# Kernel tuning notes

Hardware: AMD Instinct MI355X
Metric: run time of the kernel (lower is better)

## Reference

```python
import jax, jax.numpy as jnp
import numpy as np

INPUT_SIZE = 84 * 84 * 4  # 28224
FEATURE_SIZE = 1500
BATCH = 256

def setup_inputs() -> dict:
    key = jax.random.key(0)
    k_x, k_we, k_wd = jax.random.split(key, 3)
    scale_e = 1.0 / np.sqrt(INPUT_SIZE)
    scale_d = 1.0 / np.sqrt(FEATURE_SIZE)
    return {
        "x": jax.random.normal(k_x, (BATCH, INPUT_SIZE), dtype=jnp.float32),
        "W_enc": jax.random.normal(k_we, (FEATURE_SIZE, INPUT_SIZE), dtype=jnp.float32) * scale_e,
        "b_enc": jnp.zeros((FEATURE_SIZE,), dtype=jnp.float32),
        "W_dec": jax.random.normal(k_wd, (INPUT_SIZE, FEATURE_SIZE), dtype=jnp.float32) * scale_d,
        "b_dec": jnp.zeros((INPUT_SIZE,), dtype=jnp.float32),
    }

def reference(x, W_enc, b_enc, W_dec, b_dec):
    # Encoder: y_enc = sigmoid(x @ W_enc^T + b_enc), shape [B, F]
    y_enc = jax.nn.sigmoid(jnp.einsum('bi,fi->bf', x, W_enc) + b_enc)
    # Contractive (Jacobian Frobenius norm) term, closed form:
    # d y_enc[b,i] / d x[b,:] = y*(1-y) * W_enc[i,:]
    # jac_reg = sum_{b,i} (y*(1-y))^2 * ||W_enc[i,:]||^2
    s2 = jnp.square(y_enc * (1.0 - y_enc))          # [B, F]
    row_norm2 = jnp.sum(jnp.square(W_enc), axis=1)  # [F]
    jac_reg = jnp.sum(s2 * row_norm2)               # scalar
    # Decoder
    y_out = jax.nn.sigmoid(jnp.einsum('bf,if->bi', y_enc, W_dec) + b_dec)
    return y_out, jac_reg
```

## Files before the change

### kernel.cpp

```cpp
#include <hip/hip_runtime.h>
#include <hip/hip_bf16.h>


#define BATCH 256
#define IN    28224
#define FEAT  1500
#define FPAD  1536
#define KPAD  1504
#define ENC_S 21

typedef __attribute__((ext_vector_type(8))) short short8;
typedef __attribute__((ext_vector_type(4))) float f32x4;

__device__ __forceinline__ unsigned pack2(float lo, float hi) {
    unsigned a = __float_as_uint(lo) + 0x8000u;
    unsigned b = __float_as_uint(hi) + 0x8000u;
    return __builtin_amdgcn_perm(b, a, 0x07060302);
}
__device__ __forceinline__ unsigned short f2bf(float f) {
    unsigned u = __float_as_uint(f);
    return (unsigned short)((u + 0x7FFFu + ((u >> 16) & 1u)) >> 16);
}

__device__ __forceinline__ void async16(const unsigned short* g, unsigned short* l) {
    __builtin_amdgcn_global_load_lds(
        (const __attribute__((address_space(1))) unsigned int*)g,
        (__attribute__((address_space(3))) unsigned int*)l,
        16, 0, 0);
}


__global__ __launch_bounds__(256) void cvt_x(const float* __restrict__ x,
                                             unsigned short* __restrict__ xbf) {
    int idx = blockIdx.x * 256 + threadIdx.x;
    float4 v = ((const float4*)x)[idx];
    ((uint2*)xbf)[idx] = make_uint2(pack2(v.x, v.y), pack2(v.z, v.w));
}


__global__ __launch_bounds__(256) void enc_fused(const unsigned short* __restrict__ xbf,
                                                 const float* __restrict__ We,
                                                 float* __restrict__ part,
                                                 float* __restrict__ rn2) {
    __shared__ unsigned short As[256 * 32];
    __shared__ unsigned short Bs[64 * 32];

    const int n0 = blockIdx.x * 64;
    const int kb = blockIdx.y * 1344;
    const int t    = threadIdx.x;
    const int lane = t & 63;
    const int w    = t >> 6;
    const int l15  = lane & 15;
    const int quad = lane >> 4;

    const unsigned short* ga = xbf + (long)(w * 64 + (lane >> 2)) * IN + kb + (lane & 3) * 8;
    unsigned short* la = As + (w * 64) * 32;

    const int br = t >> 2;
    const int bf_ = n0 + br;
    const bool bvalid = bf_ < FEAT;
    const float* bsrc = We + (long)(bvalid ? bf_ : FEAT - 1) * IN + kb + (t & 3) * 8;
    unsigned short* bdst = Bs + br * 32 + (t & 3) * 8;

    float rsq = 0.f;
    f32x4 acc[4][4];
#pragma unroll
    for (int mt = 0; mt < 4; ++mt)
#pragma unroll
        for (int nt = 0; nt < 4; ++nt) { f32x4 z = {0.f,0.f,0.f,0.f}; acc[mt][nt] = z; }

    float4 v0 = *(const float4*)(bsrc);
    float4 v1 = *(const float4*)(bsrc + 4);

    for (int k = 0; k < 1344; k += 32) {
        __syncthreads();
        async16(ga + k,            la);
        async16(ga + 16 * IN + k,  la + 16 * 32);
        async16(ga + 32 * IN + k,  la + 32 * 32);
        async16(ga + 48 * IN + k,  la + 48 * 32);
        uint2 p0 = make_uint2(pack2(v0.x, v0.y), pack2(v0.z, v0.w));
        uint2 p1 = make_uint2(pack2(v1.x, v1.y), pack2(v1.z, v1.w));
        if (!bvalid) { p0 = make_uint2(0u, 0u); p1 = make_uint2(0u, 0u); }
        *(uint2*)bdst       = p0;
        *(uint2*)(bdst + 4) = p1;
        rsq += v0.x*v0.x + v0.y*v0.y + v0.z*v0.z + v0.w*v0.w
             + v1.x*v1.x + v1.y*v1.y + v1.z*v1.z + v1.w*v1.w;
        const int kn = k + 32;
        if (kn < 1344) {
            v0 = *(const float4*)(bsrc + kn);
            v1 = *(const float4*)(bsrc + kn + 4);
        }
        __syncthreads();

        short8 a[4], b[4];
#pragma unroll
        for (int mt = 0; mt < 4; ++mt)
            a[mt] = *(const short8*)(As + (w * 64 + mt * 16 + l15) * 32 + quad * 8);
#pragma unroll
        for (int nt = 0; nt < 4; ++nt)
            b[nt] = *(const short8*)(Bs + (nt * 16 + l15) * 32 + quad * 8);
#pragma unroll
        for (int mt = 0; mt < 4; ++mt)
#pragma unroll
            for (int nt = 0; nt < 4; ++nt)
                acc[mt][nt] = __builtin_amdgcn_mfma_f32_16x16x32_bf16(a[mt], b[nt], acc[mt][nt], 0, 0, 0);
    }

    float* ps = part + (long)blockIdx.y * (BATCH * FPAD);
#pragma unroll
    for (int nt = 0; nt < 4; ++nt) {
        const int col = n0 + nt * 16 + l15;
#pragma unroll
        for (int mt = 0; mt < 4; ++mt) {
            const int row = w * 64 + mt * 16 + quad * 4;
#pragma unroll
            for (int r = 0; r < 4; ++r)
                ps[(long)(row + r) * FPAD + col] = acc[mt][nt][r];
        }
    }

    rsq += __shfl_xor(rsq, 1);
    rsq += __shfl_xor(rsq, 2);
    if ((lane & 3) == 0 && bvalid) atomicAdd(&rn2[bf_], rsq);
}

__global__ __launch_bounds__(256) void act_jac_f(const float* __restrict__ part,
                                                 const float* __restrict__ be,
                                                 const float* __restrict__ rn2,
                                                 unsigned short* __restrict__ yenc,
                                                 float* __restrict__ jac) {
    const int b = blockIdx.y;
    const int f = blockIdx.x * 256 + threadIdx.x;
    float local = 0.0f;
    unsigned short h = 0;
    if (f < FEAT) {
        float p = be[f];
#pragma unroll 3
        for (int s = 0; s < ENC_S; ++s)
            p += part[(long)(s * BATCH + b) * FPAD + f];
        float y = 1.0f / (1.0f + __expf(-p));
        h = f2bf(y);
        float sg = y * (1.0f - y);
        local = sg * sg * rn2[f];
    }
    if (f < KPAD) yenc[b * KPAD + f] = h;

    float v = local;
#pragma unroll
    for (int off = 32; off > 0; off >>= 1) v += __shfl_down(v, off);
    __shared__ float red[4];
    if ((threadIdx.x & 63) == 0) red[threadIdx.x >> 6] = v;
    __syncthreads();
    if (threadIdx.x == 0) atomicAdd(jac, red[0] + red[1] + red[2] + red[3]);
}

__global__ __launch_bounds__(256) void dec_fused(const unsigned short* __restrict__ yenc,
                                                 const float* __restrict__ Wd,
                                                 const float* __restrict__ bd,
                                                 float* __restrict__ out) {
    __shared__ unsigned short As[256 * 32];
    __shared__ unsigned short Bs[64 * 32];

    const int n0 = blockIdx.x * 64;
    const int t    = threadIdx.x;
    const int lane = t & 63;
    const int w    = t >> 6;
    const int l15  = lane & 15;
    const int quad = lane >> 4;

    const unsigned short* ga = yenc + (long)(w * 64 + (lane >> 2)) * KPAD + (lane & 3) * 8;
    unsigned short* la = As + (w * 64) * 32;

    const int br = t >> 2;
    const int bn = n0 + br;
    const float* bsrc = Wd + (long)bn * FEAT + (t & 3) * 8;
    unsigned short* bdst = Bs + br * 32 + (t & 3) * 8;

    f32x4 acc[4][4];
#pragma unroll
    for (int mt = 0; mt < 4; ++mt)
#pragma unroll
        for (int nt = 0; nt < 4; ++nt) { f32x4 z = {0.f,0.f,0.f,0.f}; acc[mt][nt] = z; }

    float4 v0 = *(const float4*)(bsrc);
    float4 v1 = *(const float4*)(bsrc + 4);

    for (int k = 0; k < KPAD; k += 32) {
        __syncthreads();
        async16(ga + k,              la);
        async16(ga + 16 * KPAD + k,  la + 16 * 32);
        async16(ga + 32 * KPAD + k,  la + 32 * 32);
        async16(ga + 48 * KPAD + k,  la + 48 * 32);
        *(uint2*)bdst       = make_uint2(pack2(v0.x, v0.y), pack2(v0.z, v0.w));
        *(uint2*)(bdst + 4) = make_uint2(pack2(v1.x, v1.y), pack2(v1.z, v1.w));
        const int kn = k + 32;
        if (kn < KPAD) {
            v0 = *(const float4*)(bsrc + kn);
            const int cc = kn + (t & 3) * 8 + 4;
            if (cc + 3 < FEAT) v1 = *(const float4*)(bsrc + kn + 4);
            else               v1 = make_float4(0.f, 0.f, 0.f, 0.f);
        }
        __syncthreads();

        short8 a[4], b[4];
#pragma unroll
        for (int mt = 0; mt < 4; ++mt)
            a[mt] = *(const short8*)(As + (w * 64 + mt * 16 + l15) * 32 + quad * 8);
#pragma unroll
        for (int nt = 0; nt < 4; ++nt)
            b[nt] = *(const short8*)(Bs + (nt * 16 + l15) * 32 + quad * 8);
#pragma unroll
        for (int mt = 0; mt < 4; ++mt)
#pragma unroll
            for (int nt = 0; nt < 4; ++nt)
                acc[mt][nt] = __builtin_amdgcn_mfma_f32_16x16x32_bf16(a[mt], b[nt], acc[mt][nt], 0, 0, 0);
    }

#pragma unroll
    for (int nt = 0; nt < 4; ++nt) {
        const int col = n0 + nt * 16 + l15;
        const float bias = bd[col];
#pragma unroll
        for (int mt = 0; mt < 4; ++mt) {
            const int row = w * 64 + mt * 16 + quad * 4;
#pragma unroll
            for (int r = 0; r < 4; ++r) {
                float v = acc[mt][nt][r] + bias;
                out[(long)(row + r) * IN + col] = 1.0f / (1.0f + __expf(-v));
            }
        }
    }
}

#define LDA 40

__global__ __launch_bounds__(256) void enc_gemm(const unsigned short* __restrict__ xbf,
                                                const float* __restrict__ We,
                                                float* __restrict__ preact,
                                                float* __restrict__ rn2) {
    __shared__ unsigned short As[256 * LDA];
    __shared__ unsigned short Bs[64 * LDA];
    const int n0 = blockIdx.x * 64;
    const int kb = blockIdx.y * 672;
    const int t = threadIdx.x, lane = t & 63, w = t >> 6, l15 = lane & 15, quad = lane >> 4;
    const unsigned short* asrc = xbf + (long)(t >> 2) * IN + (t & 3) * 8 + kb;
    unsigned short* adst = As + (t >> 2) * LDA + (t & 3) * 8;
    const int brow = t >> 3, bc4 = t & 7;
    const int f0 = n0 + brow, f1 = f0 + 32;
    const float* bsrc0 = We + (long)(f0 < FEAT ? f0 : FEAT - 1) * IN + bc4 * 4 + kb;
    const float* bsrc1 = We + (long)(f1 < FEAT ? f1 : FEAT - 1) * IN + bc4 * 4 + kb;
    unsigned short* bdst0 = Bs + brow * LDA + bc4 * 4;
    unsigned short* bdst1 = bdst0 + 32 * LDA;
    float rsq0 = 0.f, rsq1 = 0.f;
    f32x4 acc[4][4];
#pragma unroll
    for (int mt = 0; mt < 4; ++mt)
#pragma unroll
        for (int nt = 0; nt < 4; ++nt) { f32x4 z = {0.f,0.f,0.f,0.f}; acc[mt][nt] = z; }
    for (int k = 0; k < 672; k += 32) {
        short8 av[4];
#pragma unroll
        for (int j = 0; j < 4; ++j) av[j] = *(const short8*)(asrc + (long)64 * j * IN + k);
        const float4 bv0 = *(const float4*)(bsrc0 + k);
        const float4 bv1 = *(const float4*)(bsrc1 + k);
        __syncthreads();
#pragma unroll
        for (int j = 0; j < 4; ++j) *(short8*)(adst + 64 * j * LDA) = av[j];
        *(uint2*)bdst0 = make_uint2(pack2(bv0.x, bv0.y), pack2(bv0.z, bv0.w));
        *(uint2*)bdst1 = make_uint2(pack2(bv1.x, bv1.y), pack2(bv1.z, bv1.w));
        rsq0 += bv0.x*bv0.x + bv0.y*bv0.y + bv0.z*bv0.z + bv0.w*bv0.w;
        rsq1 += bv1.x*bv1.x + bv1.y*bv1.y + bv1.z*bv1.z + bv1.w*bv1.w;
        __syncthreads();
        short8 a[4], b[4];
#pragma unroll
        for (int mt = 0; mt < 4; ++mt) a[mt] = *(const short8*)(As + (w * 64 + mt * 16 + l15) * LDA + quad * 8);
#pragma unroll
        for (int nt = 0; nt < 4; ++nt) b[nt] = *(const short8*)(Bs + (nt * 16 + l15) * LDA + quad * 8);
#pragma unroll
        for (int mt = 0; mt < 4; ++mt)
#pragma unroll
            for (int nt = 0; nt < 4; ++nt)
                acc[mt][nt] = __builtin_amdgcn_mfma_f32_16x16x32_bf16(a[mt], b[nt], acc[mt][nt], 0, 0, 0);
    }
#pragma unroll
    for (int nt = 0; nt < 4; ++nt) {
        const int col = n0 + nt * 16 + l15;
        if (col < FEAT) {
#pragma unroll
            for (int mt = 0; mt < 4; ++mt) {
                float* p = preact + (long)(w * 64 + mt * 16 + quad * 4) * FEAT + col;
#pragma unroll
                for (int r = 0; r < 4; ++r) atomicAdd(p + (long)r * FEAT, acc[mt][nt][r]);
            }
        }
    }
    {
        float v0 = rsq0, v1 = rsq1;
#pragma unroll
        for (int off = 1; off < 8; off <<= 1) { v0 += __shfl_xor(v0, off); v1 += __shfl_xor(v1, off); }
        if ((lane & 7) == 0) {
            if (f0 < FEAT) atomicAdd(&rn2[f0], v0);
            if (f1 < FEAT) atomicAdd(&rn2[f1], v1);
        }
    }
}

__global__ __launch_bounds__(256) void act_jac(const float* __restrict__ preact,
                                               const float* __restrict__ be,
                                               const float* __restrict__ rn2,
                                               unsigned short* __restrict__ yenc,
                                               float* __restrict__ jac) {
    const int b = blockIdx.y;
    const int f = blockIdx.x * 256 + threadIdx.x;
    float local = 0.0f;
    unsigned short h = 0;
    if (f < FEAT) {
        float p = preact[b * FEAT + f] + be[f];
        float y = 1.0f / (1.0f + __expf(-p));
        h = f2bf(y);
        float s = y * (1.0f - y);
        local = s * s * rn2[f];
    }
    yenc[b * FPAD + f] = h;
    float v = local;
#pragma unroll
    for (int off = 32; off > 0; off >>= 1) v += __shfl_down(v, off);
    __shared__ float red[4];
    if ((threadIdx.x & 63) == 0) red[threadIdx.x >> 6] = v;
    __syncthreads();
    if (threadIdx.x == 0) atomicAdd(jac, red[0] + red[1] + red[2] + red[3]);
}

__global__ __launch_bounds__(256) void dec_gemm(const unsigned short* __restrict__ yenc,
                                                const float* __restrict__ Wd,
                                                const float* __restrict__ bd,
                                                float* __restrict__ out) {
    __shared__ unsigned short As[128 * LDA];
    __shared__ unsigned short Bs[64 * LDA];
    const int m0 = (blockIdx.x & 1) * 128;
    const int n0 = (blockIdx.x >> 1) * 64;
    const int t = threadIdx.x, lane = t & 63, w = t >> 6, l15 = lane & 15, quad = lane >> 4;
    const int mrow = (w >> 1) * 64, ncol = (w & 1) * 32;
    const unsigned short* asrc = yenc + (long)(m0 + (t >> 2)) * FPAD + (t & 3) * 8;
    unsigned short* adst = As + (t >> 2) * LDA + (t & 3) * 8;
    const float* bsrc = Wd + (long)(n0 + (t >> 3)) * FEAT + (t & 7) * 4;
    unsigned short* bdst = Bs + (t >> 3) * LDA + (t & 7) * 4;
    f32x4 acc[4][2];
#pragma unroll
    for (int mt = 0; mt < 4; ++mt)
#pragma unroll
        for (int nt = 0; nt < 2; ++nt) { f32x4 z = {0.f,0.f,0.f,0.f}; acc[mt][nt] = z; }
    for (int k = 0; k < 1504; k += 32) {
        short8 av[2];
#pragma unroll
        for (int j = 0; j < 2; ++j) av[j] = *(const short8*)(asrc + (long)64 * j * FPAD + k);
        float4 bv0, bv1;
        if (k < 1472) {
            bv0 = *(const float4*)(bsrc + k);
            bv1 = *(const float4*)(bsrc + (long)32 * FEAT + k);
        } else {
            if ((t & 7) == 7) { bv0 = make_float4(0,0,0,0); bv1 = bv0; }
            else {
                bv0 = *(const float4*)(bsrc + k);
                bv1 = *(const float4*)(bsrc + (long)32 * FEAT + k);
            }
        }
        __syncthreads();
#pragma unroll
        for (int j = 0; j < 2; ++j) *(short8*)(adst + 64 * j * LDA) = av[j];
        *(uint2*)bdst = make_uint2(pack2(bv0.x, bv0.y), pack2(bv0.z, bv0.w));
        *(uint2*)(bdst + 32 * LDA) = make_uint2(pack2(bv1.x, bv1.y), pack2(bv1.z, bv1.w));
        __syncthreads();
        short8 a[4], b[2];
#pragma unroll
        for (int mt = 0; mt < 4; ++mt) a[mt] = *(const short8*)(As + (mrow + mt * 16 + l15) * LDA + quad * 8);
#pragma unroll
        for (int nt = 0; nt < 2; ++nt) b[nt] = *(const short8*)(Bs + (ncol + nt * 16 + l15) * LDA + quad * 8);
#pragma unroll
        for (int mt = 0; mt < 4; ++mt)
#pragma unroll
            for (int nt = 0; nt < 2; ++nt)
                acc[mt][nt] = __builtin_amdgcn_mfma_f32_16x16x32_bf16(a[mt], b[nt], acc[mt][nt], 0, 0, 0);
    }
#pragma unroll
    for (int nt = 0; nt < 2; ++nt) {
        const int col = n0 + ncol + nt * 16 + l15;
        const float bias = bd[col];
#pragma unroll
        for (int mt = 0; mt < 4; ++mt) {
            const int row = m0 + mrow + mt * 16 + quad * 4;
#pragma unroll
            for (int r = 0; r < 4; ++r) {
                float v = acc[mt][nt][r] + bias;
                out[(long)(row + r) * IN + col] = 1.0f / (1.0f + __expf(-v));
            }
        }
    }
}

extern "C" void kernel_launch(void* const* d_in, const int* in_sizes, int n_in,
                              void* d_out, int out_size, void* d_ws, size_t ws_size,
                              hipStream_t stream) {
    const float* x  = (const float*)d_in[0];
    const float* We = (const float*)d_in[1];
    const float* be = (const float*)d_in[2];
    const float* Wd = (const float*)d_in[3];
    const float* bd = (const float*)d_in[4];
    float* out = (float*)d_out;
    char* ws = (char*)d_ws;

    if (ws_size >= 48257024ull) {
        unsigned short* xbf  = (unsigned short*)ws;
        unsigned short* yenc = (unsigned short*)(ws + 14450688);
        float* part          = (float*)(ws + 15220736);
        float* rn2           = (float*)(ws + 48250880);

        hipMemsetAsync(rn2, 0, 6144, stream);
        hipMemsetAsync(out + 7225344, 0, 4, stream);

        cvt_x<<<7056, 256, 0, stream>>>(x, xbf);
        enc_fused<<<dim3(24, ENC_S), 256, 0, stream>>>(xbf, We, part, rn2);
        act_jac_f<<<dim3(6, 256), 256, 0, stream>>>(part, be, rn2, yenc, out + 7225344);
        dec_fused<<<441, 256, 0, stream>>>(yenc, Wd, bd, out);
    } else {
        float* preact        = (float*)ws;
        float* rn2           = (float*)(ws + 1536000);
        unsigned short* yenc = (unsigned short*)(ws + 1542144);
        unsigned short* xbf  = (unsigned short*)(ws + 2328576);

        hipMemsetAsync(ws, 0, 1542144, stream);
        hipMemsetAsync(out + 7225344, 0, 4, stream);

        cvt_x<<<7056, 256, 0, stream>>>(x, xbf);
        enc_gemm<<<dim3(24, 42), 256, 0, stream>>>(xbf, We, preact, rn2);
        act_jac<<<dim3(6, 256), 256, 0, stream>>>(preact, be, rn2, yenc, out + 7225344);
        dec_gemm<<<882, 256, 0, stream>>>(yenc, Wd, bd, out);
    }
}
```

Before: 462.8 us.

## Double-buffer encoder/decoder GEMM tiles, double split-K, halve decoder M tile

Both fused GEMM kernels move to double-buffered LDS with a k-major layout, so the next tile's loads run alongside the current MFMA work and each iteration needs one barrier instead of two. The encoder split-K factor goes from 21 to 42, giving more blocks for occupancy at the cost of a larger partial-sum buffer and more reduction work in act_jac_f. The decoder splits M into two 128-row halves, which doubles its grid to 882 blocks with smaller per-wave tiles. The fused path now needs a larger workspace, and the old path is used as a fallback when the workspace is too small.

Result: slower. 558.8 us (+20.7%).

```diff
diff --git a/kernel.cpp b/kernel.cpp
--- a/kernel.cpp
+++ b/kernel.cpp
@@ -7,7 +7,7 @@
 #define FEAT  1500
 #define FPAD  1536
 #define KPAD  1504
-#define ENC_S 21
+#define ENC_S 42
 
 typedef __attribute__((ext_vector_type(8))) short short8;
 typedef __attribute__((ext_vector_type(4))) float f32x4;
@@ -38,29 +38,32 @@
 }
 
 
-__global__ __launch_bounds__(256) void enc_fused(const unsigned short* __restrict__ xbf,
-                                                 const float* __restrict__ We,
-                                                 float* __restrict__ part,
-                                                 float* __restrict__ rn2) {
-    __shared__ unsigned short As[256 * 32];
-    __shared__ unsigned short Bs[64 * 32];
+__global__ __launch_bounds__(256, 4) void enc_fused(const unsigned short* __restrict__ xbf,
+                                                    const float* __restrict__ We,
+                                                    float* __restrict__ part,
+                                                    float* __restrict__ rn2) {
+    __shared__ unsigned short As[2 * 4 * 256 * 8];
+    __shared__ unsigned short Bs[2 * 4 * 64 * 8];
 
     const int n0 = blockIdx.x * 64;
-    const int kb = blockIdx.y * 1344;
+    const int kb = blockIdx.y * 672;
     const int t    = threadIdx.x;
     const int lane = t & 63;
     const int w    = t >> 6;
     const int l15  = lane & 15;
     const int quad = lane >> 4;
 
-    const unsigned short* ga = xbf + (long)(w * 64 + (lane >> 2)) * IN + kb + (lane & 3) * 8;
-    unsigned short* la = As + (w * 64) * 32;
-
-    const int br = t >> 2;
+    const unsigned short* gaA = xbf + (long)lane * IN + kb + w * 8;
+    unsigned short* laA = As + w * 2048;
+
+    const int br = t >> 2, sb = t & 3;
     const int bf_ = n0 + br;
     const bool bvalid = bf_ < FEAT;
-    const float* bsrc = We + (long)(bvalid ? bf_ : FEAT - 1) * IN + kb + (t & 3) * 8;
-    unsigned short* bdst = Bs + br * 32 + (t & 3) * 8;
+    const float* bsrc = We + (long)(bvalid ? bf_ : FEAT - 1) * IN + kb + sb * 8;
+    unsigned short* lbB = Bs + sb * 512 + br * 8;
+
+    const unsigned short* rdA = As + quad * 2048 + (w * 64 + l15) * 8;
+    const unsigned short* rdB = Bs + quad * 512 + l15 * 8;
 
     float rsq = 0.f;
     f32x4 acc[4][4];
@@ -71,39 +74,54 @@
 
     float4 v0 = *(const float4*)(bsrc);
     float4 v1 = *(const float4*)(bsrc + 4);
-
-    for (int k = 0; k < 1344; k += 32) {
-        __syncthreads();
-        async16(ga + k,            la);
-        async16(ga + 16 * IN + k,  la + 16 * 32);
-        async16(ga + 32 * IN + k,  la + 32 * 32);
-        async16(ga + 48 * IN + k,  la + 48 * 32);
-        uint2 p0 = make_uint2(pack2(v0.x, v0.y), pack2(v0.z, v0.w));
-        uint2 p1 = make_uint2(pack2(v1.x, v1.y), pack2(v1.z, v1.w));
-        if (!bvalid) { p0 = make_uint2(0u, 0u); p1 = make_uint2(0u, 0u); }
-        *(uint2*)bdst       = p0;
-        *(uint2*)(bdst + 4) = p1;
+#pragma unroll
+    for (int j = 0; j < 4; ++j)
+        async16(gaA + (long)j * 64 * IN, laA + j * 512);
+    {
+        uint4 p;
+        p.x = pack2(v0.x, v0.y); p.y = pack2(v0.z, v0.w);
+        p.z = pack2(v1.x, v1.y); p.w = pack2(v1.z, v1.w);
+        *(uint4*)lbB = p;
         rsq += v0.x*v0.x + v0.y*v0.y + v0.z*v0.z + v0.w*v0.w
              + v1.x*v1.x + v1.y*v1.y + v1.z*v1.z + v1.w*v1.w;
-        const int kn = k + 32;
-        if (kn < 1344) {
-            v0 = *(const float4*)(bsrc + kn);
-            v1 = *(const float4*)(bsrc + kn + 4);
-        }
-        __syncthreads();
-
+    }
+    v0 = *(const float4*)(bsrc + 32);
+    v1 = *(const float4*)(bsrc + 36);
+    __syncthreads();
+
+    int buf = 0;
+    for (int it = 0; it < 21; ++it) {
+        const int nb = buf ^ 1;
+        if (it < 20) {
+            const int kn = (it + 1) * 32;
+#pragma unroll
+            for (int j = 0; j < 4; ++j)
+                async16(gaA + (long)j * 64 * IN + kn, laA + nb * 8192 + j * 512);
+            uint4 p;
+            p.x = pack2(v0.x, v0.y); p.y = pack2(v0.z, v0.w);
+            p.z = pack2(v1.x, v1.y); p.w = pack2(v1.z, v1.w);
+            *(uint4*)(lbB + nb * 2048) = p;
+            rsq += v0.x*v0.x + v0.y*v0.y + v0.z*v0.z + v0.w*v0.w
+                 + v1.x*v1.x + v1.y*v1.y + v1.z*v1.z + v1.w*v1.w;
+            if (it < 19) {
+                v0 = *(const float4*)(bsrc + kn + 32);
+                v1 = *(const float4*)(bsrc + kn + 36);
+            }
+        }
         short8 a[4], b[4];
 #pragma unroll
         for (int mt = 0; mt < 4; ++mt)
-            a[mt] = *(const short8*)(As + (w * 64 + mt * 16 + l15) * 32 + quad * 8);
+            a[mt] = *(const short8*)(rdA + buf * 8192 + mt * 128);
 #pragma unroll
         for (int nt = 0; nt < 4; ++nt)
-            b[nt] = *(const short8*)(Bs + (nt * 16 + l15) * 32 + quad * 8);
+            b[nt] = *(const short8*)(rdB + buf * 2048 + nt * 128);
 #pragma unroll
         for (int mt = 0; mt < 4; ++mt)
 #pragma unroll
             for (int nt = 0; nt < 4; ++nt)
                 acc[mt][nt] = __builtin_amdgcn_mfma_f32_16x16x32_bf16(a[mt], b[nt], acc[mt][nt], 0, 0, 0);
+        __syncthreads();
+        buf = nb;
     }
 
     float* ps = part + (long)blockIdx.y * (BATCH * FPAD);
@@ -135,7 +153,7 @@
     unsigned short h = 0;
     if (f < FEAT) {
         float p = be[f];
-#pragma unroll 3
+#pragma unroll 6
         for (int s = 0; s < ENC_S; ++s)
             p += part[(long)(s * BATCH + b) * FPAD + f];
         float y = 1.0f / (1.0f + __expf(-p));
@@ -154,75 +172,97 @@
     if (threadIdx.x == 0) atomicAdd(jac, red[0] + red[1] + red[2] + red[3]);
 }
 
-__global__ __launch_bounds__(256) void dec_fused(const unsigned short* __restrict__ yenc,
-                                                 const float* __restrict__ Wd,
-                                                 const float* __restrict__ bd,
-                                                 float* __restrict__ out) {
-    __shared__ unsigned short As[256 * 32];
-    __shared__ unsigned short Bs[64 * 32];
-
-    const int n0 = blockIdx.x * 64;
+__global__ __launch_bounds__(256, 4) void dec_fused(const unsigned short* __restrict__ yenc,
+                                                    const float* __restrict__ Wd,
+                                                    const float* __restrict__ bd,
+                                                    float* __restrict__ out) {
+    __shared__ unsigned short As[2 * 4 * 128 * 8];
+    __shared__ unsigned short Bs[2 * 4 * 64 * 8];
+
+    const int m0 = (blockIdx.x & 1) * 128;
+    const int n0 = (blockIdx.x >> 1) * 64;
     const int t    = threadIdx.x;
     const int lane = t & 63;
     const int w    = t >> 6;
     const int l15  = lane & 15;
     const int quad = lane >> 4;
-
-    const unsigned short* ga = yenc + (long)(w * 64 + (lane >> 2)) * KPAD + (lane & 3) * 8;
-    unsigned short* la = As + (w * 64) * 32;
-
-    const int br = t >> 2;
+    const int wm   = w & 1;
+    const int wn   = w >> 1;
+
+    const unsigned short* gaA = yenc + (long)(m0 + lane) * KPAD + w * 8;
+    unsigned short* laA = As + w * 1024;
+
+    const int br = t >> 2, sb = t & 3;
     const int bn = n0 + br;
-    const float* bsrc = Wd + (long)bn * FEAT + (t & 3) * 8;
-    unsigned short* bdst = Bs + br * 32 + (t & 3) * 8;
-
-    f32x4 acc[4][4];
+    const float* bsrc = Wd + (long)bn * FEAT + sb * 8;
+    unsigned short* lbB = Bs + sb * 512 + br * 8;
+
+    const unsigned short* rdA = As + quad * 1024 + (wm * 64 + l15) * 8;
+    const unsigned short* rdB = Bs + quad * 512 + (wn * 32 + l15) * 8;
+
+    f32x4 acc[4][2];
 #pragma unroll
     for (int mt = 0; mt < 4; ++mt)
 #pragma unroll
-        for (int nt = 0; nt < 4; ++nt) { f32x4 z = {0.f,0.f,0.f,0.f}; acc[mt][nt] = z; }
+        for (int nt = 0; nt < 2; ++nt) { f32x4 z = {0.f,0.f,0.f,0.f}; acc[mt][nt] = z; }
 
     float4 v0 = *(const float4*)(bsrc);
     float4 v1 = *(const float4*)(bsrc + 4);
-
-    for (int k = 0; k < KPAD; k += 32) {
-        __syncthreads();
-        async16(ga + k,              la);
-        async16(ga + 16 * KPAD + k,  la + 16 * 32);
-        async16(ga + 32 * KPAD + k,  la + 32 * 32);
-        async16(ga + 48 * KPAD + k,  la + 48 * 32);
-        *(uint2*)bdst       = make_uint2(pack2(v0.x, v0.y), pack2(v0.z, v0.w));
-        *(uint2*)(bdst + 4) = make_uint2(pack2(v1.x, v1.y), pack2(v1.z, v1.w));
-        const int kn = k + 32;
-        if (kn < KPAD) {
-            v0 = *(const float4*)(bsrc + kn);
-            const int cc = kn + (t & 3) * 8 + 4;
-            if (cc + 3 < FEAT) v1 = *(const float4*)(bsrc + kn + 4);
-            else               v1 = make_float4(0.f, 0.f, 0.f, 0.f);
-        }
-        __syncthreads();
-
-        short8 a[4], b[4];
-#pragma unroll
-        for (int mt = 0; mt < 4; ++mt)
-            a[mt] = *(const short8*)(As + (w * 64 + mt * 16 + l15) * 32 + quad * 8);
-#pragma unroll
-        for (int nt = 0; nt < 4; ++nt)
-            b[nt] = *(const short8*)(Bs + (nt * 16 + l15) * 32 + quad * 8);
-#pragma unroll
-        for (int mt = 0; mt < 4; ++mt)
-#pragma unroll
-            for (int nt = 0; nt < 4; ++nt)
+#pragma unroll
+    for (int j = 0; j < 2; ++j)
+        async16(gaA + (long)j * 64 * KPAD, laA + j * 512);
+    {
+        uint4 p;
+        p.x = pack2(v0.x, v0.y); p.y = pack2(v0.z, v0.w);
+        p.z = pack2(v1.x, v1.y); p.w = pack2(v1.z, v1.w);
+        *(uint4*)lbB = p;
+    }
+    v0 = *(const float4*)(bsrc + 32);
+    v1 = *(const float4*)(bsrc + 36);
+    __syncthreads();
+
+    int buf = 0;
+    for (int it = 0; it < 47; ++it) {
+        const int nb = buf ^ 1;
+        if (it < 46) {
+            const int kn = (it + 1) * 32;
+#pragma unroll
+            for (int j = 0; j < 2; ++j)
+                async16(gaA + (long)j * 64 * KPAD + kn, laA + nb * 4096 + j * 512);
+            uint4 p;
+            p.x = pack2(v0.x, v0.y); p.y = pack2(v0.z, v0.w);
+            p.z = pack2(v1.x, v1.y); p.w = pack2(v1.z, v1.w);
+            *(uint4*)(lbB + nb * 2048) = p;
+            if (it < 45) {
+                const int kn2 = kn + 32;
+                v0 = *(const float4*)(bsrc + kn2);
+                if (kn2 + sb * 8 + 7 < FEAT) v1 = *(const float4*)(bsrc + kn2 + 4);
+                else                         v1 = make_float4(0.f, 0.f, 0.f, 0.f);
+            }
+        }
+        short8 a[4], b[2];
+#pragma unroll
+        for (int mt = 0; mt < 4; ++mt)
+            a[mt] = *(const short8*)(rdA + buf * 4096 + mt * 128);
+#pragma unroll
+        for (int nt = 0; nt < 2; ++nt)
+            b[nt] = *(const short8*)(rdB + buf * 2048 + nt * 128);
+#pragma unroll
+        for (int mt = 0; mt < 4; ++mt)
+#pragma unroll
+            for (int nt = 0; nt < 2; ++nt)
                 acc[mt][nt] = __builtin_amdgcn_mfma_f32_16x16x32_bf16(a[mt], b[nt], acc[mt][nt], 0, 0, 0);
-    }
-
-#pragma unroll
-    for (int nt = 0; nt < 4; ++nt) {
-        const int col = n0 + nt * 16 + l15;
+        __syncthreads();
+        buf = nb;
+    }
+
+#pragma unroll
+    for (int nt = 0; nt < 2; ++nt) {
+        const int col = n0 + wn * 32 + nt * 16 + l15;
         const float bias = bd[col];
 #pragma unroll
         for (int mt = 0; mt < 4; ++mt) {
-            const int row = w * 64 + mt * 16 + quad * 4;
+            const int row = m0 + wm * 64 + mt * 16 + quad * 4;
 #pragma unroll
             for (int r = 0; r < 4; ++r) {
                 float v = acc[mt][nt][r] + bias;
@@ -409,11 +449,11 @@
     float* out = (float*)d_out;
     char* ws = (char*)d_ws;
 
-    if (ws_size >= 48257024ull) {
+    if (ws_size >= 81287168ull) {
         unsigned short* xbf  = (unsigned short*)ws;
         unsigned short* yenc = (unsigned short*)(ws + 14450688);
         float* part          = (float*)(ws + 15220736);
-        float* rn2           = (float*)(ws + 48250880);
+        float* rn2           = (float*)(ws + 81281024);
 
         hipMemsetAsync(rn2, 0, 6144, stream);
         hipMemsetAsync(out + 7225344, 0, 4, stream);
@@ -421,7 +461,7 @@
         cvt_x<<<7056, 256, 0, stream>>>(x, xbf);
         enc_fused<<<dim3(24, ENC_S), 256, 0, stream>>>(xbf, We, part, rn2);
         act_jac_f<<<dim3(6, 256), 256, 0, stream>>>(part, be, rn2, yenc, out + 7225344);
-        dec_fused<<<441, 256, 0, stream>>>(yenc, Wd, bd, out);
+        dec_fused<<<882, 256, 0, stream>>>(yenc, Wd, bd, out);
     } else {
         float* preact        = (float*)ws;
         float* rn2           = (float*)(ws + 1536000);
```

## Replace LDS-staged GEMMs with register-streamed double-buffered MFMA loads

Applied to the files above, without the earlier changes.

Encoder and decoder GEMMs drop shared-memory staging and __syncthreads. Each lane now loads its MFMA fragments straight from global memory into registers, converting to bf16 there, with two register buffers so loads overlap compute. The encoder split-K doubles to 42 slices and the decoder tile narrows to 32 columns with twice as many blocks, to raise parallelism. The cost is redundant global loads across waves (each wave reloads the B tile), more partial-sum traffic, and a larger workspace requirement that could send execution down the fallback path.

Measured after the change: 676.6 us. +46.2%, slower.

```diff
diff --git a/kernel.cpp b/kernel.cpp
--- a/kernel.cpp
+++ b/kernel.cpp
@@ -7,7 +7,7 @@
 #define FEAT  1500
 #define FPAD  1536
 #define KPAD  1504
-#define ENC_S 21
+#define ENC_S 42
 
 typedef __attribute__((ext_vector_type(8))) short short8;
 typedef __attribute__((ext_vector_type(4))) float f32x4;
@@ -21,12 +21,13 @@
     unsigned u = __float_as_uint(f);
     return (unsigned short)((u + 0x7FFFu + ((u >> 16) & 1u)) >> 16);
 }
-
-__device__ __forceinline__ void async16(const unsigned short* g, unsigned short* l) {
-    __builtin_amdgcn_global_load_lds(
-        (const __attribute__((address_space(1))) unsigned int*)g,
-        (__attribute__((address_space(3))) unsigned int*)l,
-        16, 0, 0);
+__device__ __forceinline__ short8 packs8(float4 lo, float4 hi) {
+    union { unsigned u[4]; short8 s; } U;
+    U.u[0] = pack2(lo.x, lo.y);
+    U.u[1] = pack2(lo.z, lo.w);
+    U.u[2] = pack2(hi.x, hi.y);
+    U.u[3] = pack2(hi.z, hi.w);
+    return U.s;
 }
 
 
@@ -38,73 +39,98 @@
 }
 
 
-__global__ __launch_bounds__(256) void enc_fused(const unsigned short* __restrict__ xbf,
-                                                 const float* __restrict__ We,
-                                                 float* __restrict__ part,
-                                                 float* __restrict__ rn2) {
-    __shared__ unsigned short As[256 * 32];
-    __shared__ unsigned short Bs[64 * 32];
-
+struct EncFrag { short8 a0, a1, a2, a3, b0, b1, b2, b3; };
+struct EncStage { float4 p0, p1, p2, p3, p4, p5, p6, p7; };
+
+__device__ __forceinline__ void enc_loadA(EncFrag& F, const unsigned short* A0, int k) {
+    F.a0 = *(const short8*)(A0 + k);
+    F.a1 = *(const short8*)(A0 + 16 * IN + k);
+    F.a2 = *(const short8*)(A0 + 32 * IN + k);
+    F.a3 = *(const short8*)(A0 + 48 * IN + k);
+}
+__device__ __forceinline__ void enc_loadB(EncStage& S, const float* b0, const float* b1,
+                                          const float* b2, const float* b3, int k) {
+    S.p0 = *(const float4*)(b0 + k); S.p1 = *(const float4*)(b0 + k + 4);
+    S.p2 = *(const float4*)(b1 + k); S.p3 = *(const float4*)(b1 + k + 4);
+    S.p4 = *(const float4*)(b2 + k); S.p5 = *(const float4*)(b2 + k + 4);
+    S.p6 = *(const float4*)(b3 + k); S.p7 = *(const float4*)(b3 + k + 4);
+}
+__device__ __forceinline__ float dot8(float4 a, float4 b) {
+    return a.x*a.x + a.y*a.y + a.z*a.z + a.w*a.w
+         + b.x*b.x + b.y*b.y + b.z*b.z + b.w*b.w;
+}
+__device__ __forceinline__ void enc_cvtB(EncFrag& F, const EncStage& S, bool dosq,
+                                         float& r0, float& r1, float& r2, float& r3) {
+    F.b0 = packs8(S.p0, S.p1);
+    F.b1 = packs8(S.p2, S.p3);
+    F.b2 = packs8(S.p4, S.p5);
+    F.b3 = packs8(S.p6, S.p7);
+    if (dosq) {
+        r0 += dot8(S.p0, S.p1);
+        r1 += dot8(S.p2, S.p3);
+        r2 += dot8(S.p4, S.p5);
+        r3 += dot8(S.p6, S.p7);
+    }
+}
+__device__ __forceinline__ void enc_mfma(f32x4 (&acc)[4][4], const EncFrag& F) {
+    short8 A[4] = {F.a0, F.a1, F.a2, F.a3};
+    short8 B[4] = {F.b0, F.b1, F.b2, F.b3};
+#pragma unroll
+    for (int mt = 0; mt < 4; ++mt)
+#pragma unroll
+        for (int nt = 0; nt < 4; ++nt)
+            acc[mt][nt] = __builtin_amdgcn_mfma_f32_16x16x32_bf16(A[mt], B[nt], acc[mt][nt], 0, 0, 0);
+}
+
+__global__ __launch_bounds__(256) void enc_stream(const unsigned short* __restrict__ xbf,
+                                                  const float* __restrict__ We,
+                                                  float* __restrict__ part,
+                                                  float* __restrict__ rn2) {
     const int n0 = blockIdx.x * 64;
-    const int kb = blockIdx.y * 1344;
+    const int kb = blockIdx.y * 672;
     const int t    = threadIdx.x;
     const int lane = t & 63;
     const int w    = t >> 6;
     const int l15  = lane & 15;
     const int quad = lane >> 4;
 
-    const unsigned short* ga = xbf + (long)(w * 64 + (lane >> 2)) * IN + kb + (lane & 3) * 8;
-    unsigned short* la = As + (w * 64) * 32;
-
-    const int br = t >> 2;
-    const int bf_ = n0 + br;
-    const bool bvalid = bf_ < FEAT;
-    const float* bsrc = We + (long)(bvalid ? bf_ : FEAT - 1) * IN + kb + (t & 3) * 8;
-    unsigned short* bdst = Bs + br * 32 + (t & 3) * 8;
-
-    float rsq = 0.f;
+    const unsigned short* A0 = xbf + (long)(w * 64 + l15) * IN + kb + quad * 8;
+
+    const int rb0 = n0 + 0  + l15, rb1 = n0 + 16 + l15;
+    const int rb2 = n0 + 32 + l15, rb3 = n0 + 48 + l15;
+    const float* b0p = We + (long)(rb0 < FEAT ? rb0 : FEAT - 1) * IN + kb + quad * 8;
+    const float* b1p = We + (long)(rb1 < FEAT ? rb1 : FEAT - 1) * IN + kb + quad * 8;
+    const float* b2p = We + (long)(rb2 < FEAT ? rb2 : FEAT - 1) * IN + kb + quad * 8;
+    const float* b3p = We + (long)(rb3 < FEAT ? rb3 : FEAT - 1) * IN + kb + quad * 8;
+
+    const bool dosq = (w == 0);
+    float r0 = 0.f, r1 = 0.f, r2 = 0.f, r3 = 0.f;
+
     f32x4 acc[4][4];
 #pragma unroll
     for (int mt = 0; mt < 4; ++mt)
 #pragma unroll
         for (int nt = 0; nt < 4; ++nt) { f32x4 z = {0.f,0.f,0.f,0.f}; acc[mt][nt] = z; }
 
-    float4 v0 = *(const float4*)(bsrc);
-    float4 v1 = *(const float4*)(bsrc + 4);
-
-    for (int k = 0; k < 1344; k += 32) {
-        __syncthreads();
-        async16(ga + k,            la);
-        async16(ga + 16 * IN + k,  la + 16 * 32);
-        async16(ga + 32 * IN + k,  la + 32 * 32);
-        async16(ga + 48 * IN + k,  la + 48 * 32);
-        uint2 p0 = make_uint2(pack2(v0.x, v0.y), pack2(v0.z, v0.w));
-        uint2 p1 = make_uint2(pack2(v1.x, v1.y), pack2(v1.z, v1.w));
-        if (!bvalid) { p0 = make_uint2(0u, 0u); p1 = make_uint2(0u, 0u); }
-        *(uint2*)bdst       = p0;
-        *(uint2*)(bdst + 4) = p1;
-        rsq += v0.x*v0.x + v0.y*v0.y + v0.z*v0.z + v0.w*v0.w
-             + v1.x*v1.x + v1.y*v1.y + v1.z*v1.z + v1.w*v1.w;
-        const int kn = k + 32;
-        if (kn < 1344) {
-            v0 = *(const float4*)(bsrc + kn);
-            v1 = *(const float4*)(bsrc + kn + 4);
-        }
-        __syncthreads();
-
-        short8 a[4], b[4];
-#pragma unroll
-        for (int mt = 0; mt < 4; ++mt)
-            a[mt] = *(const short8*)(As + (w * 64 + mt * 16 + l15) * 32 + quad * 8);
-#pragma unroll
-        for (int nt = 0; nt < 4; ++nt)
-            b[nt] = *(const short8*)(Bs + (nt * 16 + l15) * 32 + quad * 8);
-#pragma unroll
-        for (int mt = 0; mt < 4; ++mt)
-#pragma unroll
-            for (int nt = 0; nt < 4; ++nt)
-                acc[mt][nt] = __builtin_amdgcn_mfma_f32_16x16x32_bf16(a[mt], b[nt], acc[mt][nt], 0, 0, 0);
-    }
+    EncFrag F0, F1; EncStage S;
+    enc_loadA(F0, A0, 0);
+    enc_loadB(S, b0p, b1p, b2p, b3p, 0);
+    enc_cvtB(F0, S, dosq, r0, r1, r2, r3);
+
+#pragma unroll 1
+    for (int p = 0; p < 10; ++p) {
+        const int k1 = (2 * p + 1) * 32;
+        const int k2 = (2 * p + 2) * 32;
+        enc_loadA(F1, A0, k1);
+        enc_loadB(S, b0p, b1p, b2p, b3p, k1);
+        enc_mfma(acc, F0);
+        enc_cvtB(F1, S, dosq, r0, r1, r2, r3);
+        enc_loadA(F0, A0, k2);
+        enc_loadB(S, b0p, b1p, b2p, b3p, k2);
+        enc_mfma(acc, F1);
+        enc_cvtB(F0, S, dosq, r0, r1, r2, r3);
+    }
+    enc_mfma(acc, F0);
 
     float* ps = part + (long)blockIdx.y * (BATCH * FPAD);
 #pragma unroll
@@ -119,9 +145,16 @@
         }
     }
 
-    rsq += __shfl_xor(rsq, 1);
-    rsq += __shfl_xor(rsq, 2);
-    if ((lane & 3) == 0 && bvalid) atomicAdd(&rn2[bf_], rsq);
+    r0 += __shfl_xor(r0, 16); r0 += __shfl_xor(r0, 32);
+    r1 += __shfl_xor(r1, 16); r1 += __shfl_xor(r1, 32);
+    r2 += __shfl_xor(r2, 16); r2 += __shfl_xor(r2, 32);
+    r3 += __shfl_xor(r3, 16); r3 += __shfl_xor(r3, 32);
+    if (dosq && lane < 16) {
+        if (rb0 < FEAT) atomicAdd(&rn2[rb0], r0);
+        if (rb1 < FEAT) atomicAdd(&rn2[rb1], r1);
+        if (rb2 < FEAT) atomicAdd(&rn2[rb2], r2);
+        if (rb3 < FEAT) atomicAdd(&rn2[rb3], r3);
+    }
 }
 
 __global__ __launch_bounds__(256) void act_jac_f(const float* __restrict__ part,
@@ -135,7 +168,7 @@
     unsigned short h = 0;
     if (f < FEAT) {
         float p = be[f];
-#pragma unroll 3
+#pragma unroll 6
         for (int s = 0; s < ENC_S; ++s)
             p += part[(long)(s * BATCH + b) * FPAD + f];
         float y = 1.0f / (1.0f + __expf(-p));
@@ -154,70 +187,86 @@
     if (threadIdx.x == 0) atomicAdd(jac, red[0] + red[1] + red[2] + red[3]);
 }
 
-__global__ __launch_bounds__(256) void dec_fused(const unsigned short* __restrict__ yenc,
-                                                 const float* __restrict__ Wd,
-                                                 const float* __restrict__ bd,
-                                                 float* __restrict__ out) {
-    __shared__ unsigned short As[256 * 32];
-    __shared__ unsigned short Bs[64 * 32];
-
-    const int n0 = blockIdx.x * 64;
+struct DecFrag { short8 a0, a1, a2, a3, b0, b1; };
+struct DecStage { float4 p0, p1, p2, p3; };
+
+__device__ __forceinline__ void dec_loadA(DecFrag& F, const unsigned short* A0, int k) {
+    F.a0 = *(const short8*)(A0 + k);
+    F.a1 = *(const short8*)(A0 + 16 * KPAD + k);
+    F.a2 = *(const short8*)(A0 + 32 * KPAD + k);
+    F.a3 = *(const short8*)(A0 + 48 * KPAD + k);
+}
+__device__ __forceinline__ void dec_loadB(DecStage& S, const float* b0, const float* b1,
+                                          const float* WdEnd, int k) {
+    S.p0 = *(const float4*)(b0 + k);
+    const float* q0 = b0 + k + 4;
+    if (q0 + 4 > WdEnd) q0 = WdEnd - 4;
+    S.p1 = *(const float4*)q0;
+    S.p2 = *(const float4*)(b1 + k);
+    const float* q1 = b1 + k + 4;
+    if (q1 + 4 > WdEnd) q1 = WdEnd - 4;
+    S.p3 = *(const float4*)q1;
+}
+__device__ __forceinline__ void dec_cvtB(DecFrag& F, const DecStage& S) {
+    F.b0 = packs8(S.p0, S.p1);
+    F.b1 = packs8(S.p2, S.p3);
+}
+__device__ __forceinline__ void dec_mfma(f32x4 (&acc)[4][2], const DecFrag& F) {
+    short8 A[4] = {F.a0, F.a1, F.a2, F.a3};
+    short8 B[2] = {F.b0, F.b1};
+#pragma unroll
+    for (int mt = 0; mt < 4; ++mt)
+#pragma unroll
+        for (int nt = 0; nt < 2; ++nt)
+            acc[mt][nt] = __builtin_amdgcn_mfma_f32_16x16x32_bf16(A[mt], B[nt], acc[mt][nt], 0, 0, 0);
+}
+
+__global__ __launch_bounds__(256) void dec_stream(const unsigned short* __restrict__ yenc,
+                                                  const float* __restrict__ Wd,
+                                                  const float* __restrict__ bd,
+                                                  float* __restrict__ out) {
+    const int n0 = blockIdx.x * 32;
     const int t    = threadIdx.x;
     const int lane = t & 63;
     const int w    = t >> 6;
     const int l15  = lane & 15;
     const int quad = lane >> 4;
 
-    const unsigned short* ga = yenc + (long)(w * 64 + (lane >> 2)) * KPAD + (lane & 3) * 8;
-    unsigned short* la = As + (w * 64) * 32;
-
-    const int br = t >> 2;
-    const int bn = n0 + br;
-    const float* bsrc = Wd + (long)bn * FEAT + (t & 3) * 8;
-    unsigned short* bdst = Bs + br * 32 + (t & 3) * 8;
-
-    f32x4 acc[4][4];
-#pragma unroll
-    for (int mt = 0; mt < 4; ++mt)
-#pragma unroll
-        for (int nt = 0; nt < 4; ++nt) { f32x4 z = {0.f,0.f,0.f,0.f}; acc[mt][nt] = z; }
-
-    float4 v0 = *(const float4*)(bsrc);
-    float4 v1 = *(const float4*)(bsrc + 4);
-
-    for (int k = 0; k < KPAD; k += 32) {
-        __syncthreads();
-        async16(ga + k,              la);
-        async16(ga + 16 * KPAD + k,  la + 16 * 32);
-        async16(ga + 32 * KPAD + k,  la + 32 * 32);
-        async16(ga + 48 * KPAD + k,  la + 48 * 32);
-        *(uint2*)bdst       = make_uint2(pack2(v0.x, v0.y), pack2(v0.z, v0.w));
-        *(uint2*)(bdst + 4) = make_uint2(pack2(v1.x, v1.y), pack2(v1.z, v1.w));
-        const int kn = k + 32;
-        if (kn < KPAD) {
-            v0 = *(const float4*)(bsrc + kn);
-            const int cc = kn + (t & 3) * 8 + 4;
-            if (cc + 3 < FEAT) v1 = *(const float4*)(bsrc + kn + 4);
-            else               v1 = make_float4(0.f, 0.f, 0.f, 0.f);
-        }
-        __syncthreads();
-
-        short8 a[4], b[4];
-#pragma unroll
-        for (int mt = 0; mt < 4; ++mt)
-            a[mt] = *(const short8*)(As + (w * 64 + mt * 16 + l15) * 32 + quad * 8);
-#pragma unroll
-        for (int nt = 0; nt < 4; ++nt)
-            b[nt] = *(const short8*)(Bs + (nt * 16 + l15) * 32 + quad * 8);
-#pragma unroll
-        for (int mt = 0; mt < 4; ++mt)
-#pragma unroll
-            for (int nt = 0; nt < 4; ++nt)
-                acc[mt][nt] = __builtin_amdgcn_mfma_f32_16x16x32_bf16(a[mt], b[nt], acc[mt][nt], 0, 0, 0);
-    }
-
-#pragma unroll
-    for (int nt = 0; nt < 4; ++nt) {
+    const unsigned short* A0 = yenc + (long)(w * 64 + l15) * KPAD + quad * 8;
+
+    const int rb0 = n0 + l15, rb1 = n0 + 16 + l15;
+    const float* b0p = Wd + (long)rb0 * FEAT + quad * 8;
+    const float* b1p = Wd + (long)rb1 * FEAT + quad * 8;
+    const float* WdEnd = Wd + (long)IN * FEAT;
+
+    f32x4 acc[4][2];
+#pragma unroll
+    for (int mt = 0; mt < 4; ++mt)
+#pragma unroll
+        for (int nt = 0; nt < 2; ++nt) { f32x4 z = {0.f,0.f,0.f,0.f}; acc[mt][nt] = z; }
+
+    DecFrag F0, F1; DecStage S;
+    dec_loadA(F0, A0, 0);
+    dec_loadB(S, b0p, b1p, WdEnd, 0);
+    dec_cvtB(F0, S);
+
+#pragma unroll 1
+    for (int p = 0; p < 23; ++p) {
+        const int k1 = (2 * p + 1) * 32;
+        const int k2 = (2 * p + 2) * 32;
+        dec_loadA(F1, A0, k1);
+        dec_loadB(S, b0p, b1p, WdEnd, k1);
+        dec_mfma(acc, F0);
+        dec_cvtB(F1, S);
+        dec_loadA(F0, A0, k2);
+        dec_loadB(S, b0p, b1p, WdEnd, k2);
+        dec_mfma(acc, F1);
+        dec_cvtB(F0, S);
+    }
+    dec_mfma(acc, F0);
+
+#pragma unroll
+    for (int nt = 0; nt < 2; ++nt) {
         const int col = n0 + nt * 16 + l15;
         const float bias = bd[col];
 #pragma unroll
@@ -409,19 +458,19 @@
     float* out = (float*)d_out;
     char* ws = (char*)d_ws;
 
-    if (ws_size >= 48257024ull) {
+    if (ws_size >= 81287168ull) {
         unsigned short* xbf  = (unsigned short*)ws;
         unsigned short* yenc = (unsigned short*)(ws + 14450688);
         float* part          = (float*)(ws + 15220736);
-        float* rn2           = (float*)(ws + 48250880);
+        float* rn2           = (float*)(ws + 81281024);
 
         hipMemsetAsync(rn2, 0, 6144, stream);
         hipMemsetAsync(out + 7225344, 0, 4, stream);
 
         cvt_x<<<7056, 256, 0, stream>>>(x, xbf);
-        enc_fused<<<dim3(24, ENC_S), 256, 0, stream>>>(xbf, We, part, rn2);
+        enc_stream<<<dim3(24, ENC_S), 256, 0, stream>>>(xbf, We, part, rn2);
         act_jac_f<<<dim3(6, 256), 256, 0, stream>>>(part, be, rn2, yenc, out + 7225344);
-        dec_fused<<<441, 256, 0, stream>>>(yenc, Wd, bd, out);
+        dec_stream<<<882, 256, 0, stream>>>(yenc, Wd, bd, out);
     } else {
         float* preact        = (float*)ws;
         float* rn2           = (float*)(ws + 1536000);
```
